# Kernel tuning notes

Measured on AMD Instinct MI355X. Metric: run time of the kernel, lower is better.

## Reference

```python
import jax, jax.numpy as jnp
import numpy as np

K = 1024      # num_embeddings
D = 256       # embedding_dim
BETA = 0.25
DECAY = 0.99
EPS = 1e-05


def setup_inputs() -> dict:
    key = jax.random.key(0)
    k1, k2 = jax.random.split(key)
    z_e = jax.random.normal(k1, (32, D, 32, 32), dtype=jnp.float32)
    embedding = jax.random.normal(k2, (K, D), dtype=jnp.float32)
    ema_cluster_size = jnp.zeros((K,), dtype=jnp.float32)
    ema_w = embedding  # buffer initialized as a clone of the codebook
    return {"z_e": z_e, "embedding": embedding,
            "ema_cluster_size": ema_cluster_size, "ema_w": ema_w}


def reference(z_e, embedding, ema_cluster_size, ema_w):
    B, Dd, H, W = z_e.shape
    # (B, D, H, W) -> (N, D)
    flat_z = jnp.transpose(z_e, (0, 2, 3, 1)).reshape(-1, Dd)

    # L2 distance argmin (||z||^2 + ||e||^2 - 2 z.e)
    dist = (jnp.sum(flat_z * flat_z, axis=1, keepdims=True)
            + jnp.sum(embedding * embedding, axis=1)
            - 2.0 * flat_z @ embedding.T)
    indices = jnp.argmin(dist, axis=1)  # (N,)

    # EMA update (operates on detached values; buffers updated in-place in torch)
    flat_z_sg = jax.lax.stop_gradient(flat_z)
    cluster_size = jax.ops.segment_sum(
        jnp.ones_like(indices, dtype=z_e.dtype), indices, num_segments=K)
    new_ema_cluster_size = DECAY * ema_cluster_size + (1.0 - DECAY) * cluster_size
    dw = jax.ops.segment_sum(flat_z_sg, indices, num_segments=K)  # one_hot.T @ flat_z
    new_ema_w = DECAY * ema_w + (1.0 - DECAY) * dw
    new_embedding = new_ema_w / (new_ema_cluster_size + EPS)[:, None]

    # Gather uses the *updated* codebook (torch copies into the buffer first)
    z_q_flat = new_embedding[indices]                      # (N, D)
    z_q = jnp.transpose(z_q_flat.reshape(B, H, W, Dd), (0, 3, 1, 2))

    # Straight-through estimator + commitment loss
    z_q_st = z_e + jax.lax.stop_gradient(z_q - z_e)
    vq_loss = BETA * jnp.mean((z_e - jax.lax.stop_gradient(z_q)) ** 2)

    return (z_q_st, vq_loss, indices.reshape(B, H, W),
            new_embedding, new_ema_cluster_size, new_ema_w)
```

## Files before the change

### kernel.cpp

```cpp
#include <hip/hip_runtime.h>
#include <stdint.h>

#define N_ROWS 32768
#define K_CODES 1024
#define D_DIM 256
#define NELEM 8388608

#define WS_COUNTS 0
#define WS_ENORM 263168
#define WS_ROWBEST_BYTES 1056768
#define WS_IDX_BYTES 1318912

#define O_ZQ 0
#define O_LOSS 8388608
#define O_IDX 8388609
#define O_EMB 8421377
#define O_CS 8683521
#define O_EMAW 8684545

#define EP_BYTE_OFF 33685520

typedef _Float16 half8 __attribute__((ext_vector_type(8)));
typedef float f32x16 __attribute__((ext_vector_type(16)));

__device__ __forceinline__ unsigned int fenc(float f) {
    unsigned int u = __float_as_uint(f);
    return (u & 0x80000000u) ? ~u : (u | 0x80000000u);
}
__device__ __forceinline__ unsigned long long umin64(unsigned long long a, unsigned long long b) {
    return a < b ? a : b;
}
__device__ __forceinline__ void gll16(const void* g, void* l) {
    __builtin_amdgcn_global_load_lds((const __attribute__((address_space(1))) void*)g,
                                     (__attribute__((address_space(3))) void*)l, 16, 0, 0);
}

__global__ __launch_bounds__(256) void k_init(float* ws) {
    int i = blockIdx.x * 256 + threadIdx.x;
    if (i < 1024) ws[i] = 0.0f;
    unsigned long long* rb = (unsigned long long*)((char*)ws + WS_ROWBEST_BYTES);
    if (i < N_ROWS) rb[i] = 0xFFFFFFFFFFFFFFFFull;
}

__global__ __launch_bounds__(256) void k_conv_e(const float* __restrict__ emb,
                                                _Float16* __restrict__ Ep,
                                                float* __restrict__ enorm) {
    int k = blockIdx.x, d = threadIdx.x;
    float v = emb[k * 256 + d];
    _Float16 h = (_Float16)v;
    _Float16 l = (_Float16)(v - (float)h);
    int s = d >> 3, sub = d & 7;
    Ep[((size_t)s * 1024 + k) * 8 + sub] = h;
    Ep[((size_t)(32 + s) * 1024 + k) * 8 + sub] = l;
    float sq = v * v;
    #pragma unroll
    for (int off = 32; off >= 1; off >>= 1) sq += __shfl_down(sq, off, 64);
    __shared__ float red[4];
    if ((d & 63) == 0) red[d >> 6] = sq;
    __syncthreads();
    if (d == 0) enorm[k] = (red[0] + red[1]) + (red[2] + red[3]);
}

__global__ __launch_bounds__(256) void k_conv_z(const float* __restrict__ z_e,
                                                _Float16* __restrict__ Zp) {
    __shared__ float lt[64 * 68];
    int t = threadIdx.x;
    int hw0 = blockIdx.x * 64, d0 = blockIdx.y * 64, b = blockIdx.z;
    const float* src = z_e + (size_t)b * 262144 + (size_t)d0 * 1024 + hw0;
    int dl = t >> 4, hl = (t & 15) * 4;
    #pragma unroll
    for (int i = 0; i < 4; i++) {
        int d = dl + i * 16;
        float4 v = *(const float4*)(src + (size_t)d * 1024 + hl);
        lt[(hl + 0) * 68 + d] = v.x;
        lt[(hl + 1) * 68 + d] = v.y;
        lt[(hl + 2) * 68 + d] = v.z;
        lt[(hl + 3) * 68 + d] = v.w;
    }
    __syncthreads();
    int hr = t >> 2, seg = t & 3;
    int n = b * 1024 + hw0 + hr;
    int sg0 = (d0 >> 3) + seg * 2;
    half8 hi[2], lo[2];
    #pragma unroll
    for (int p = 0; p < 2; p++) {
        #pragma unroll
        for (int j = 0; j < 8; j++) {
            float v = lt[hr * 68 + seg * 16 + p * 8 + j];
            _Float16 h = (_Float16)v;
            hi[p][j] = h;
            lo[p][j] = (_Float16)(v - (float)h);
        }
    }
    *(half8*)(Zp + ((size_t)(sg0 + 0) * 32768 + n) * 8) = hi[0];
    *(half8*)(Zp + ((size_t)(sg0 + 1) * 32768 + n) * 8) = hi[1];
    *(half8*)(Zp + ((size_t)(32 + sg0) * 32768 + n) * 8) = lo[0];
    *(half8*)(Zp + ((size_t)(33 + sg0) * 32768 + n) * 8) = lo[1];
}

__global__ __launch_bounds__(256) void k_mm(const _Float16* __restrict__ Zp,
                                            const _Float16* __restrict__ Ep,
                                            const float* __restrict__ enorm,
                                            unsigned long long* __restrict__ row_best) {
    __shared__ __align__(16) char smem[32768];
    _Float16* Za = (_Float16*)smem;
    _Float16* Ea = (_Float16*)(smem + 16384);
    unsigned long long* slot = (unsigned long long*)smem;

    int t = threadIdx.x;
    int lane = t & 63, wv = t >> 6;
    int b = blockIdx.x;
    int rt = (b & 7) + ((b >> 6) << 3);
    int ct = (b >> 3) & 7;
    int row0 = rt * 128, code0 = ct * 128;

    int wr = wv >> 1, wc = wv & 1;
    int m31 = lane & 31, ko = lane >> 5;

    f32x16 acc[2][2];
    #pragma unroll
    for (int i = 0; i < 2; i++)
        #pragma unroll
        for (int j = 0; j < 2; j++)
            #pragma unroll
            for (int r = 0; r < 16; r++) acc[i][j][r] = 0.0f;

    const char* zgl = (const char*)Zp + ((size_t)(2 * wv) * 32768 + row0 + lane) * 16;
    const char* egl = (const char*)Ep + ((size_t)(2 * wv) * 1024 + code0 + lane) * 16;
    _Float16* zld = Za + (2 * wv) * 1024;
    _Float16* eld = Ea + (2 * wv) * 1024;

    for (int c = 0; c < 12; c++) {
        int kz = (c < 8) ? c : (c - 8);
        int ge = (c < 4) ? c * 8 : (c < 8) ? (c - 4) * 8 : 32 + (c - 8) * 8;
        const char* zg = zgl + (size_t)kz * 8 * 32768 * 16;
        const char* eg = egl + (size_t)ge * 1024 * 16;
        gll16(zg, zld);
        gll16(zg + 64 * 16, zld + 512);
        gll16(zg + 32768 * 16, zld + 1024);
        gll16(zg + 32768 * 16 + 64 * 16, zld + 1536);
        gll16(eg, eld);
        gll16(eg + 64 * 16, eld + 512);
        gll16(eg + 1024 * 16, eld + 1024);
        gll16(eg + 1024 * 16 + 64 * 16, eld + 1536);
        __syncthreads();
        #pragma unroll
        for (int ks = 0; ks < 4; ks++) {
            int sseg = 2 * ks + ko;
            half8 a0 = *(const half8*)(Za + sseg * 1024 + (wr * 64 + m31) * 8);
            half8 a1 = *(const half8*)(Za + sseg * 1024 + (wr * 64 + 32 + m31) * 8);
            half8 b0 = *(const half8*)(Ea + sseg * 1024 + (wc * 64 + m31) * 8);
            half8 b1 = *(const half8*)(Ea + sseg * 1024 + (wc * 64 + 32 + m31) * 8);
            acc[0][0] = __builtin_amdgcn_mfma_f32_32x32x16_f16(a0, b0, acc[0][0], 0, 0, 0);
            acc[0][1] = __builtin_amdgcn_mfma_f32_32x32x16_f16(a0, b1, acc[0][1], 0, 0, 0);
            acc[1][0] = __builtin_amdgcn_mfma_f32_32x32x16_f16(a1, b0, acc[1][0], 0, 0, 0);
            acc[1][1] = __builtin_amdgcn_mfma_f32_32x32x16_f16(a1, b1, acc[1][1], 0, 0, 0);
        }
        __syncthreads();
    }

    float en0 = enorm[code0 + wc * 64 + m31];
    float en1 = enorm[code0 + wc * 64 + 32 + m31];
    unsigned int col0 = code0 + wc * 64 + m31;
    unsigned int col1 = col0 + 32;

    if (wc == 0) {
        #pragma unroll
        for (int mt = 0; mt < 2; mt++)
            #pragma unroll
            for (int j = 0; j < 16; j++) {
                int row = wr * 64 + mt * 32 + 4 * ko + (j & 3) + 8 * (j >> 2);
                unsigned long long p0 = ((unsigned long long)fenc(en0 - 2.0f * acc[mt][0][j]) << 32) | col0;
                unsigned long long p1 = ((unsigned long long)fenc(en1 - 2.0f * acc[mt][1][j]) << 32) | col1;
                slot[row * 32 + ((m31 + row) & 31)] = umin64(p0, p1);
            }
    }
    __syncthreads();
    if (wc == 1) {
        #pragma unroll
        for (int mt = 0; mt < 2; mt++)
            #pragma unroll
            for (int j = 0; j < 16; j++) {
                int row = wr * 64 + mt * 32 + 4 * ko + (j & 3) + 8 * (j >> 2);
                unsigned long long p0 = ((unsigned long long)fenc(en0 - 2.0f * acc[mt][0][j]) << 32) | col0;
                unsigned long long p1 = ((unsigned long long)fenc(en1 - 2.0f * acc[mt][1][j]) << 32) | col1;
                atomicMin(&slot[row * 32 + ((m31 + row) & 31)], umin64(p0, p1));
            }
    }
    __syncthreads();
    if (t < 128) {
        unsigned long long m = slot[t * 32 + (t & 31)];
        #pragma unroll
        for (int i = 1; i < 32; i++) m = umin64(m, slot[t * 32 + ((i + t) & 31)]);
        atomicMin(&row_best[row0 + t], m);
    }
}

__global__ __launch_bounds__(256) void k_fin_idx(const unsigned long long* __restrict__ rb,
                                                 int* __restrict__ idxs, float* __restrict__ out) {
    int i = blockIdx.x * 256 + threadIdx.x;
    if (i < N_ROWS) {
        int id = (int)(rb[i] & 0xFFFFFFFFull);
        idxs[i] = id;
        out[O_IDX + i] = (float)id;
    }
}

__global__ __launch_bounds__(256) void k_counts(const int* __restrict__ idxs,
                                                float* __restrict__ counts) {
    __shared__ float hist[K_CODES];
    int t = threadIdx.x;
    #pragma unroll
    for (int j = 0; j < 4; j++) hist[j * 256 + t] = 0.0f;
    __syncthreads();
    int n0 = blockIdx.x * 1024;
    #pragma unroll
    for (int i = 0; i < 4; i++) {
        int id = idxs[n0 + i * 256 + t];
        atomicAdd(&hist[id], 1.0f);
    }
    __syncthreads();
    #pragma unroll
    for (int j = 0; j < 4; j++) {
        float h = hist[j * 256 + t];
        if (h != 0.0f) atomicAdd(&counts[j * 256 + t], h);
    }
}

__global__ __launch_bounds__(256) void k_dw(const float* __restrict__ z_e,
                                            const int* __restrict__ idxs,
                                            float* __restrict__ part) {
    __shared__ float acc[K_CODES];
    int t = threadIdx.x;
    int s = blockIdx.x;
    int d = blockIdx.y;
    #pragma unroll
    for (int j = 0; j < 4; j++) acc[j * 256 + t] = 0.0f;
    __syncthreads();
    #pragma unroll
    for (int i = 0; i < 4; i++) {
        int b = s * 4 + i;
        int4 id4 = *(const int4*)(idxs + b * 1024 + t * 4);
        float4 v = *(const float4*)(z_e + (size_t)b * 262144 + (size_t)d * 1024 + t * 4);
        atomicAdd(&acc[id4.x], v.x);
        atomicAdd(&acc[id4.y], v.y);
        atomicAdd(&acc[id4.z], v.z);
        atomicAdd(&acc[id4.w], v.w);
    }
    __syncthreads();
    float* pr = part + ((size_t)s * 256 + d) * 1024;
    #pragma unroll
    for (int j = 0; j < 4; j++) pr[j * 256 + t] = acc[j * 256 + t];
}

__global__ __launch_bounds__(256) void k_red(const float* __restrict__ part,
                                             const float* __restrict__ ema_cs,
                                             const float* __restrict__ ema_w,
                                             const float* __restrict__ counts,
                                             float* __restrict__ out) {
    __shared__ float tile[64 * 69];
    __shared__ float csl[64];
    int t = threadIdx.x;
    int k0 = blockIdx.x * 64, d0 = blockIdx.y * 64;
    int dr = t >> 4, kc = t & 15;
    float4 sum[4] = {};
    for (int s = 0; s < 8; s++) {
        const float* pb = part + ((size_t)s * 256 + d0) * 1024 + k0 + kc * 4;
        #pragma unroll
        for (int q = 0; q < 4; q++) {
            float4 v = *(const float4*)(pb + (size_t)(dr + 16 * q) * 1024);
            sum[q].x += v.x; sum[q].y += v.y; sum[q].z += v.z; sum[q].w += v.w;
        }
    }
    if (t < 64) csl[t] = 0.99f * ema_cs[k0 + t] + 0.01f * counts[k0 + t];
    #pragma unroll
    for (int q = 0; q < 4; q++) {
        float* p = tile + (dr + 16 * q) * 69 + kc * 4;
        p[0] = sum[q].x; p[1] = sum[q].y; p[2] = sum[q].z; p[3] = sum[q].w;
    }
    __syncthreads();
    int kk = t >> 2, dq = t & 3;
    int k = k0 + kk;
    float inv = 1.0f / (csl[kk] + 1e-5f);
    #pragma unroll
    for (int j4 = 0; j4 < 4; j4++) {
        int dd = dq * 16 + j4 * 4;
        size_t kd = (size_t)k * 256 + d0 + dd;
        float4 w = *(const float4*)(ema_w + kd);
        float4 nw;
        nw.x = 0.99f * w.x + 0.01f * tile[(dd + 0) * 69 + kk];
        nw.y = 0.99f * w.y + 0.01f * tile[(dd + 1) * 69 + kk];
        nw.z = 0.99f * w.z + 0.01f * tile[(dd + 2) * 69 + kk];
        nw.w = 0.99f * w.w + 0.01f * tile[(dd + 3) * 69 + kk];
        *(float4*)(out + O_EMAW + kd) = nw;
        float4 ne = {nw.x * inv, nw.y * inv, nw.z * inv, nw.w * inv};
        *(float4*)(out + O_EMB + kd) = ne;
    }
    if (blockIdx.y == 0 && t < 64) out[O_CS + k0 + t] = csl[t];
    if (blockIdx.x == 0 && blockIdx.y == 0 && t == 0) out[O_LOSS] = 0.0f;
}

__global__ __launch_bounds__(256) void k_gather(const float* __restrict__ z_e,
                                                const int* __restrict__ idxs,
                                                float* __restrict__ out) {
    __shared__ float lt[64 * 68];
    __shared__ int sid[64];
    __shared__ float red[4];
    int t = threadIdx.x;
    int hw0 = blockIdx.x * 64, d0 = blockIdx.y * 64, b = blockIdx.z;
    if (t < 64) sid[t] = idxs[b * 1024 + hw0 + t];
    const float* src = z_e + (size_t)b * 262144 + (size_t)d0 * 1024 + hw0;
    int dl = t >> 4, hl = (t & 15) * 4;
    #pragma unroll
    for (int i = 0; i < 4; i++) {
        int d = dl + i * 16;
        float4 v = *(const float4*)(src + (size_t)d * 1024 + hl);
        lt[(hl + 0) * 68 + d] = v.x;
        lt[(hl + 1) * 68 + d] = v.y;
        lt[(hl + 2) * 68 + d] = v.z;
        lt[(hl + 3) * 68 + d] = v.w;
    }
    __syncthreads();
    int r = t >> 2, c = t & 3;
    const float* nrow = out + O_EMB + (size_t)sid[r] * 256 + d0;
    float lacc = 0.0f;
    #pragma unroll
    for (int it = 0; it < 4; it++) {
        int dd = it * 16 + c * 4;
        float4 q = *(const float4*)(nrow + dd);
        float* p = lt + r * 68 + dd;
        float z0 = p[0], z1 = p[1], z2 = p[2], z3 = p[3];
        p[0] = z0 + (q.x - z0);
        p[1] = z1 + (q.y - z1);
        p[2] = z2 + (q.z - z2);
        p[3] = z3 + (q.w - z3);
        float dx = z0 - q.x, dy = z1 - q.y, dz = z2 - q.z, dw4 = z3 - q.w;
        lacc += dx * dx + dy * dy + dz * dz + dw4 * dw4;
    }
    __syncthreads();
    float* dst = out + O_ZQ + (size_t)b * 262144 + (size_t)d0 * 1024 + hw0;
    #pragma unroll
    for (int i = 0; i < 4; i++) {
        int d = dl + i * 16;
        float4 w;
        w.x = lt[(hl + 0) * 68 + d];
        w.y = lt[(hl + 1) * 68 + d];
        w.z = lt[(hl + 2) * 68 + d];
        w.w = lt[(hl + 3) * 68 + d];
        *(float4*)(dst + (size_t)d * 1024 + hl) = w;
    }
    #pragma unroll
    for (int off = 32; off >= 1; off >>= 1) lacc += __shfl_down(lacc, off, 64);
    int lane = t & 63, wv = t >> 6;
    if (lane == 0) red[wv] = lacc;
    __syncthreads();
    if (t == 0) {
        float s = (red[0] + red[1]) + (red[2] + red[3]);
        atomicAdd(out + O_LOSS, s * 2.9802322387695312e-08f);
    }
}

extern "C" void kernel_launch(void* const* d_in, const int* in_sizes, int n_in,
                              void* d_out, int out_size, void* d_ws, size_t ws_size,
                              hipStream_t stream) {
    const float* z_e = (const float*)d_in[0];
    const float* emb = (const float*)d_in[1];
    const float* ema_cs = (const float*)d_in[2];
    const float* ema_w = (const float*)d_in[3];
    float* out = (float*)d_out;
    float* ws = (float*)d_ws;

    float* counts = ws + WS_COUNTS;
    float* enorm = ws + WS_ENORM;
    unsigned long long* row_best = (unsigned long long*)((char*)d_ws + WS_ROWBEST_BYTES);
    int* idxs = (int*)((char*)d_ws + WS_IDX_BYTES);

    _Float16* Zp = (_Float16*)d_out;
    _Float16* Ep = (_Float16*)((char*)d_out + EP_BYTE_OFF);
    float* part = (float*)d_out;

    k_init<<<128, 256, 0, stream>>>(ws);
    k_conv_e<<<1024, 256, 0, stream>>>(emb, Ep, enorm);
    k_conv_z<<<dim3(16, 4, 32), 256, 0, stream>>>(z_e, Zp);
    k_mm<<<2048, 256, 0, stream>>>(Zp, Ep, enorm, row_best);
    k_fin_idx<<<128, 256, 0, stream>>>(row_best, idxs, out);
    k_counts<<<32, 256, 0, stream>>>(idxs, counts);
    k_dw<<<dim3(8, 256), 256, 0, stream>>>(z_e, idxs, part);
    k_red<<<dim3(16, 4), 256, 0, stream>>>(part, ema_cs, ema_w, counts, out);
    k_gather<<<dim3(16, 4, 32), 256, 0, stream>>>(z_e, idxs, out);
}
```

Before: 255.0 us.

## Drop LDS staging in distance GEMM; load fragments directly with register prefetch

```diff
diff --git a/kernel.cpp b/kernel.cpp
--- a/kernel.cpp
+++ b/kernel.cpp
@@ -29,10 +29,6 @@
 }
 __device__ __forceinline__ unsigned long long umin64(unsigned long long a, unsigned long long b) {
     return a < b ? a : b;
-}
-__device__ __forceinline__ void gll16(const void* g, void* l) {
-    __builtin_amdgcn_global_load_lds((const __attribute__((address_space(1))) void*)g,
-                                     (__attribute__((address_space(3))) void*)l, 16, 0, 0);
 }
 
 __global__ __launch_bounds__(256) void k_init(float* ws) {
@@ -102,20 +98,20 @@
                                             const _Float16* __restrict__ Ep,
                                             const float* __restrict__ enorm,
                                             unsigned long long* __restrict__ row_best) {
-    __shared__ __align__(16) char smem[32768];
-    _Float16* Za = (_Float16*)smem;
-    _Float16* Ea = (_Float16*)(smem + 16384);
-    unsigned long long* slot = (unsigned long long*)smem;
-
     int t = threadIdx.x;
     int lane = t & 63, wv = t >> 6;
     int b = blockIdx.x;
-    int rt = (b & 7) + ((b >> 6) << 3);
-    int ct = (b >> 3) & 7;
-    int row0 = rt * 128, code0 = ct * 128;
-
-    int wr = wv >> 1, wc = wv & 1;
+    int rt = (b & 7) + ((b >> 7) << 3);
+    int ct = (b >> 3) & 15;
+    int row0 = rt * 256 + wv * 64;
+    int code0 = ct * 64;
     int m31 = lane & 31, ko = lane >> 5;
+
+    const char* ebase = (const char*)Ep + ((size_t)ko * 1024 + code0 + m31) * 16;
+    const char* zbase = (const char*)Zp + ((size_t)ko * 32768 + row0 + m31) * 16;
+
+    constexpr int ZB[12] = {0, 8, 16, 24, 32, 40, 48, 56, 0, 8, 16, 24};
+    constexpr int EB[12] = {0, 8, 16, 24, 0, 8, 16, 24, 32, 40, 48, 56};
 
     f32x16 acc[2][2];
     #pragma unroll
@@ -125,74 +121,49 @@
             #pragma unroll
             for (int r = 0; r < 16; r++) acc[i][j][r] = 0.0f;
 
-    const char* zgl = (const char*)Zp + ((size_t)(2 * wv) * 32768 + row0 + lane) * 16;
-    const char* egl = (const char*)Ep + ((size_t)(2 * wv) * 1024 + code0 + lane) * 16;
-    _Float16* zld = Za + (2 * wv) * 1024;
-    _Float16* eld = Ea + (2 * wv) * 1024;
-
-    for (int c = 0; c < 12; c++) {
-        int kz = (c < 8) ? c : (c - 8);
-        int ge = (c < 4) ? c * 8 : (c < 8) ? (c - 4) * 8 : 32 + (c - 8) * 8;
-        const char* zg = zgl + (size_t)kz * 8 * 32768 * 16;
-        const char* eg = egl + (size_t)ge * 1024 * 16;
-        gll16(zg, zld);
-        gll16(zg + 64 * 16, zld + 512);
-        gll16(zg + 32768 * 16, zld + 1024);
-        gll16(zg + 32768 * 16 + 64 * 16, zld + 1536);
-        gll16(eg, eld);
-        gll16(eg + 64 * 16, eld + 512);
-        gll16(eg + 1024 * 16, eld + 1024);
-        gll16(eg + 1024 * 16 + 64 * 16, eld + 1536);
-        __syncthreads();
-        #pragma unroll
-        for (int ks = 0; ks < 4; ks++) {
-            int sseg = 2 * ks + ko;
-            half8 a0 = *(const half8*)(Za + sseg * 1024 + (wr * 64 + m31) * 8);
-            half8 a1 = *(const half8*)(Za + sseg * 1024 + (wr * 64 + 32 + m31) * 8);
-            half8 b0 = *(const half8*)(Ea + sseg * 1024 + (wc * 64 + m31) * 8);
-            half8 b1 = *(const half8*)(Ea + sseg * 1024 + (wc * 64 + 32 + m31) * 8);
-            acc[0][0] = __builtin_amdgcn_mfma_f32_32x32x16_f16(a0, b0, acc[0][0], 0, 0, 0);
-            acc[0][1] = __builtin_amdgcn_mfma_f32_32x32x16_f16(a0, b1, acc[0][1], 0, 0, 0);
-            acc[1][0] = __builtin_amdgcn_mfma_f32_32x32x16_f16(a1, b0, acc[1][0], 0, 0, 0);
-            acc[1][1] = __builtin_amdgcn_mfma_f32_32x32x16_f16(a1, b1, acc[1][1], 0, 0, 0);
+#define LDA(c, s, mt) (*(const half8*)(ebase + (((size_t)(EB[c] + 2 * (s))) * 1024 + (mt) * 32) * 16))
+#define LDB(c, s, nt) (*(const half8*)(zbase + (((size_t)(ZB[c] + 2 * (s))) * 32768 + (nt) * 32) * 16))
+
+    half8 a0 = LDA(0, 0, 0), a1 = LDA(0, 0, 1);
+    half8 b0 = LDB(0, 0, 0), b1 = LDB(0, 0, 1);
+    #pragma unroll
+    for (int i = 0; i < 48; i++) {
+        half8 na0, na1, nb0, nb1;
+        if (i < 47) {
+            int c2 = (i + 1) >> 2, s2 = (i + 1) & 3;
+            na0 = LDA(c2, s2, 0); na1 = LDA(c2, s2, 1);
+            nb0 = LDB(c2, s2, 0); nb1 = LDB(c2, s2, 1);
         }
-        __syncthreads();
-    }
-
-    float en0 = enorm[code0 + wc * 64 + m31];
-    float en1 = enorm[code0 + wc * 64 + 32 + m31];
-    unsigned int col0 = code0 + wc * 64 + m31;
-    unsigned int col1 = col0 + 32;
-
-    if (wc == 0) {
+        acc[0][0] = __builtin_amdgcn_mfma_f32_32x32x16_f16(a0, b0, acc[0][0], 0, 0, 0);
+        acc[0][1] = __builtin_amdgcn_mfma_f32_32x32x16_f16(a0, b1, acc[0][1], 0, 0, 0);
+        acc[1][0] = __builtin_amdgcn_mfma_f32_32x32x16_f16(a1, b0, acc[1][0], 0, 0, 0);
+        acc[1][1] = __builtin_amdgcn_mfma_f32_32x32x16_f16(a1, b1, acc[1][1], 0, 0, 0);
+        a0 = na0; a1 = na1; b0 = nb0; b1 = nb1;
+    }
+#undef LDA
+#undef LDB
+
+    float en_a[32];
+    #pragma unroll
+    for (int mt = 0; mt < 2; mt++)
+        #pragma unroll
+        for (int r = 0; r < 16; r++)
+            en_a[mt * 16 + r] = enorm[code0 + mt * 32 + 4 * ko + (r & 3) + 8 * (r >> 2)];
+
+    #pragma unroll
+    for (int nt = 0; nt < 2; nt++) {
+        unsigned long long best = 0xFFFFFFFFFFFFFFFFull;
         #pragma unroll
         for (int mt = 0; mt < 2; mt++)
             #pragma unroll
-            for (int j = 0; j < 16; j++) {
-                int row = wr * 64 + mt * 32 + 4 * ko + (j & 3) + 8 * (j >> 2);
-                unsigned long long p0 = ((unsigned long long)fenc(en0 - 2.0f * acc[mt][0][j]) << 32) | col0;
-                unsigned long long p1 = ((unsigned long long)fenc(en1 - 2.0f * acc[mt][1][j]) << 32) | col1;
-                slot[row * 32 + ((m31 + row) & 31)] = umin64(p0, p1);
+            for (int r = 0; r < 16; r++) {
+                unsigned int code = code0 + mt * 32 + 4 * ko + (r & 3) + 8 * (r >> 2);
+                float dist = en_a[mt * 16 + r] - 2.0f * acc[mt][nt][r];
+                unsigned long long pk = ((unsigned long long)fenc(dist) << 32) | code;
+                best = umin64(best, pk);
             }
-    }
-    __syncthreads();
-    if (wc == 1) {
-        #pragma unroll
-        for (int mt = 0; mt < 2; mt++)
-            #pragma unroll
-            for (int j = 0; j < 16; j++) {
-                int row = wr * 64 + mt * 32 + 4 * ko + (j & 3) + 8 * (j >> 2);
-                unsigned long long p0 = ((unsigned long long)fenc(en0 - 2.0f * acc[mt][0][j]) << 32) | col0;
-                unsigned long long p1 = ((unsigned long long)fenc(en1 - 2.0f * acc[mt][1][j]) << 32) | col1;
-                atomicMin(&slot[row * 32 + ((m31 + row) & 31)], umin64(p0, p1));
-            }
-    }
-    __syncthreads();
-    if (t < 128) {
-        unsigned long long m = slot[t * 32 + (t & 31)];
-        #pragma unroll
-        for (int i = 1; i < 32; i++) m = umin64(m, slot[t * 32 + ((i + t) & 31)]);
-        atomicMin(&row_best[row0 + t], m);
+        best = umin64(best, __shfl_xor(best, 32, 64));
+        if (ko == 0) atomicMin(&row_best[row0 + nt * 32 + m31], best);
     }
 }
 
```

New measurement: 277.4 us. 1.09x slower.

## Compute commitment loss algebraically and drop z_e reread in gather

Applied to the files above, without the earlier changes.

```diff
diff --git a/kernel.cpp b/kernel.cpp
--- a/kernel.cpp
+++ b/kernel.cpp
@@ -7,6 +7,7 @@
 #define NELEM 8388608
 
 #define WS_COUNTS 0
+#define WS_LOSS 1030
 #define WS_ENORM 263168
 #define WS_ROWBEST_BYTES 1056768
 #define WS_IDX_BYTES 1318912
@@ -37,7 +38,7 @@
 
 __global__ __launch_bounds__(256) void k_init(float* ws) {
     int i = blockIdx.x * 256 + threadIdx.x;
-    if (i < 1024) ws[i] = 0.0f;
+    if (i < 2048) ws[i] = 0.0f;
     unsigned long long* rb = (unsigned long long*)((char*)ws + WS_ROWBEST_BYTES);
     if (i < N_ROWS) rb[i] = 0xFFFFFFFFFFFFFFFFull;
 }
@@ -62,16 +63,20 @@
 }
 
 __global__ __launch_bounds__(256) void k_conv_z(const float* __restrict__ z_e,
-                                                _Float16* __restrict__ Zp) {
+                                                _Float16* __restrict__ Zp,
+                                                float* __restrict__ lossacc) {
     __shared__ float lt[64 * 68];
+    __shared__ float red[4];
     int t = threadIdx.x;
     int hw0 = blockIdx.x * 64, d0 = blockIdx.y * 64, b = blockIdx.z;
     const float* src = z_e + (size_t)b * 262144 + (size_t)d0 * 1024 + hw0;
     int dl = t >> 4, hl = (t & 15) * 4;
+    float sq = 0.0f;
     #pragma unroll
     for (int i = 0; i < 4; i++) {
         int d = dl + i * 16;
         float4 v = *(const float4*)(src + (size_t)d * 1024 + hl);
+        sq += v.x * v.x + v.y * v.y + v.z * v.z + v.w * v.w;
         lt[(hl + 0) * 68 + d] = v.x;
         lt[(hl + 1) * 68 + d] = v.y;
         lt[(hl + 2) * 68 + d] = v.z;
@@ -96,6 +101,11 @@
     *(half8*)(Zp + ((size_t)(sg0 + 1) * 32768 + n) * 8) = hi[1];
     *(half8*)(Zp + ((size_t)(32 + sg0) * 32768 + n) * 8) = lo[0];
     *(half8*)(Zp + ((size_t)(33 + sg0) * 32768 + n) * 8) = lo[1];
+    #pragma unroll
+    for (int off = 32; off >= 1; off >>= 1) sq += __shfl_down(sq, off, 64);
+    if ((t & 63) == 0) red[t >> 6] = sq;
+    __syncthreads();
+    if (t == 0) atomicAdd(lossacc, (red[0] + red[1]) + (red[2] + red[3]));
 }
 
 __global__ __launch_bounds__(256) void k_mm(const _Float16* __restrict__ Zp,
@@ -127,8 +137,8 @@
 
     const char* zgl = (const char*)Zp + ((size_t)(2 * wv) * 32768 + row0 + lane) * 16;
     const char* egl = (const char*)Ep + ((size_t)(2 * wv) * 1024 + code0 + lane) * 16;
-    _Float16* zld = Za + (2 * wv) * 1024;
-    _Float16* eld = Ea + (2 * wv) * 1024;
+    _Float16* zld = Za + 2 * wv * 1024;
+    _Float16* eld = Ea + 2 * wv * 1024;
 
     for (int c = 0; c < 12; c++) {
         int kz = (c < 8) ? c : (c - 8);
@@ -197,28 +207,19 @@
 }
 
 __global__ __launch_bounds__(256) void k_fin_idx(const unsigned long long* __restrict__ rb,
-                                                 int* __restrict__ idxs, float* __restrict__ out) {
-    int i = blockIdx.x * 256 + threadIdx.x;
-    if (i < N_ROWS) {
-        int id = (int)(rb[i] & 0xFFFFFFFFull);
-        idxs[i] = id;
-        out[O_IDX + i] = (float)id;
-    }
-}
-
-__global__ __launch_bounds__(256) void k_counts(const int* __restrict__ idxs,
-                                                float* __restrict__ counts) {
+                                                 int* __restrict__ idxs,
+                                                 float* __restrict__ counts,
+                                                 float* __restrict__ out) {
     __shared__ float hist[K_CODES];
     int t = threadIdx.x;
     #pragma unroll
     for (int j = 0; j < 4; j++) hist[j * 256 + t] = 0.0f;
     __syncthreads();
-    int n0 = blockIdx.x * 1024;
-    #pragma unroll
-    for (int i = 0; i < 4; i++) {
-        int id = idxs[n0 + i * 256 + t];
-        atomicAdd(&hist[id], 1.0f);
-    }
+    int i = blockIdx.x * 256 + t;
+    int id = (int)(rb[i] & 0xFFFFFFFFull);
+    idxs[i] = id;
+    out[O_IDX + i] = (float)id;
+    atomicAdd(&hist[id], 1.0f);
     __syncthreads();
     #pragma unroll
     for (int j = 0; j < 4; j++) {
@@ -257,9 +258,12 @@
                                              const float* __restrict__ ema_cs,
                                              const float* __restrict__ ema_w,
                                              const float* __restrict__ counts,
+                                             float* __restrict__ lossacc,
                                              float* __restrict__ out) {
     __shared__ float tile[64 * 69];
     __shared__ float csl[64];
+    __shared__ float craw[64];
+    __shared__ float red[4];
     int t = threadIdx.x;
     int k0 = blockIdx.x * 64, d0 = blockIdx.y * 64;
     int dr = t >> 4, kc = t & 15;
@@ -272,7 +276,11 @@
             sum[q].x += v.x; sum[q].y += v.y; sum[q].z += v.z; sum[q].w += v.w;
         }
     }
-    if (t < 64) csl[t] = 0.99f * ema_cs[k0 + t] + 0.01f * counts[k0 + t];
+    if (t < 64) {
+        float c = counts[k0 + t];
+        craw[t] = c;
+        csl[t] = 0.99f * ema_cs[k0 + t] + 0.01f * c;
+    }
     #pragma unroll
     for (int q = 0; q < 4; q++) {
         float* p = tile + (dr + 16 * q) * 69 + kc * 4;
@@ -282,62 +290,58 @@
     int kk = t >> 2, dq = t & 3;
     int k = k0 + kk;
     float inv = 1.0f / (csl[kk] + 1e-5f);
+    float cr = craw[kk];
+    float lterm = 0.0f;
     #pragma unroll
     for (int j4 = 0; j4 < 4; j4++) {
         int dd = dq * 16 + j4 * 4;
         size_t kd = (size_t)k * 256 + d0 + dd;
         float4 w = *(const float4*)(ema_w + kd);
+        float s0 = tile[(dd + 0) * 69 + kk];
+        float s1 = tile[(dd + 1) * 69 + kk];
+        float s2 = tile[(dd + 2) * 69 + kk];
+        float s3 = tile[(dd + 3) * 69 + kk];
         float4 nw;
-        nw.x = 0.99f * w.x + 0.01f * tile[(dd + 0) * 69 + kk];
-        nw.y = 0.99f * w.y + 0.01f * tile[(dd + 1) * 69 + kk];
-        nw.z = 0.99f * w.z + 0.01f * tile[(dd + 2) * 69 + kk];
-        nw.w = 0.99f * w.w + 0.01f * tile[(dd + 3) * 69 + kk];
+        nw.x = 0.99f * w.x + 0.01f * s0;
+        nw.y = 0.99f * w.y + 0.01f * s1;
+        nw.z = 0.99f * w.z + 0.01f * s2;
+        nw.w = 0.99f * w.w + 0.01f * s3;
         *(float4*)(out + O_EMAW + kd) = nw;
         float4 ne = {nw.x * inv, nw.y * inv, nw.z * inv, nw.w * inv};
         *(float4*)(out + O_EMB + kd) = ne;
+        lterm += ne.x * (cr * ne.x - 2.0f * s0);
+        lterm += ne.y * (cr * ne.y - 2.0f * s1);
+        lterm += ne.z * (cr * ne.z - 2.0f * s2);
+        lterm += ne.w * (cr * ne.w - 2.0f * s3);
     }
     if (blockIdx.y == 0 && t < 64) out[O_CS + k0 + t] = csl[t];
-    if (blockIdx.x == 0 && blockIdx.y == 0 && t == 0) out[O_LOSS] = 0.0f;
-}
-
-__global__ __launch_bounds__(256) void k_gather(const float* __restrict__ z_e,
-                                                const int* __restrict__ idxs,
-                                                float* __restrict__ out) {
+    #pragma unroll
+    for (int off = 32; off >= 1; off >>= 1) lterm += __shfl_down(lterm, off, 64);
+    if ((t & 63) == 0) red[t >> 6] = lterm;
+    __syncthreads();
+    if (t == 0) atomicAdd(lossacc, (red[0] + red[1]) + (red[2] + red[3]));
+}
+
+__global__ __launch_bounds__(256) void k_bcast(const int* __restrict__ idxs,
+                                               const float* __restrict__ lossacc,
+                                               float* __restrict__ out) {
     __shared__ float lt[64 * 68];
     __shared__ int sid[64];
-    __shared__ float red[4];
     int t = threadIdx.x;
     int hw0 = blockIdx.x * 64, d0 = blockIdx.y * 64, b = blockIdx.z;
     if (t < 64) sid[t] = idxs[b * 1024 + hw0 + t];
-    const float* src = z_e + (size_t)b * 262144 + (size_t)d0 * 1024 + hw0;
-    int dl = t >> 4, hl = (t & 15) * 4;
-    #pragma unroll
-    for (int i = 0; i < 4; i++) {
-        int d = dl + i * 16;
-        float4 v = *(const float4*)(src + (size_t)d * 1024 + hl);
-        lt[(hl + 0) * 68 + d] = v.x;
-        lt[(hl + 1) * 68 + d] = v.y;
-        lt[(hl + 2) * 68 + d] = v.z;
-        lt[(hl + 3) * 68 + d] = v.w;
-    }
     __syncthreads();
     int r = t >> 2, c = t & 3;
     const float* nrow = out + O_EMB + (size_t)sid[r] * 256 + d0;
-    float lacc = 0.0f;
     #pragma unroll
     for (int it = 0; it < 4; it++) {
         int dd = it * 16 + c * 4;
         float4 q = *(const float4*)(nrow + dd);
         float* p = lt + r * 68 + dd;
-        float z0 = p[0], z1 = p[1], z2 = p[2], z3 = p[3];
-        p[0] = z0 + (q.x - z0);
-        p[1] = z1 + (q.y - z1);
-        p[2] = z2 + (q.z - z2);
-        p[3] = z3 + (q.w - z3);
-        float dx = z0 - q.x, dy = z1 - q.y, dz = z2 - q.z, dw4 = z3 - q.w;
-        lacc += dx * dx + dy * dy + dz * dz + dw4 * dw4;
-    }
-    __syncthreads();
+        p[0] = q.x; p[1] = q.y; p[2] = q.z; p[3] = q.w;
+    }
+    __syncthreads();
+    int dl = t >> 4, hl = (t & 15) * 4;
     float* dst = out + O_ZQ + (size_t)b * 262144 + (size_t)d0 * 1024 + hw0;
     #pragma unroll
     for (int i = 0; i < 4; i++) {
@@ -349,15 +353,8 @@
         w.w = lt[(hl + 3) * 68 + d];
         *(float4*)(dst + (size_t)d * 1024 + hl) = w;
     }
-    #pragma unroll
-    for (int off = 32; off >= 1; off >>= 1) lacc += __shfl_down(lacc, off, 64);
-    int lane = t & 63, wv = t >> 6;
-    if (lane == 0) red[wv] = lacc;
-    __syncthreads();
-    if (t == 0) {
-        float s = (red[0] + red[1]) + (red[2] + red[3]);
-        atomicAdd(out + O_LOSS, s * 2.9802322387695312e-08f);
-    }
+    if (blockIdx.x == 0 && blockIdx.y == 0 && blockIdx.z == 0 && t == 0)
+        out[O_LOSS] = lossacc[0] * 2.9802322387695312e-08f;
 }
 
 extern "C" void kernel_launch(void* const* d_in, const int* in_sizes, int n_in,
@@ -371,6 +368,7 @@
     float* ws = (float*)d_ws;
 
     float* counts = ws + WS_COUNTS;
+    float* lossacc = ws + WS_LOSS;
     float* enorm = ws + WS_ENORM;
     unsigned long long* row_best = (unsigned long long*)((char*)d_ws + WS_ROWBEST_BYTES);
     int* idxs = (int*)((char*)d_ws + WS_IDX_BYTES);
@@ -381,11 +379,10 @@
 
     k_init<<<128, 256, 0, stream>>>(ws);
     k_conv_e<<<1024, 256, 0, stream>>>(emb, Ep, enorm);
-    k_conv_z<<<dim3(16, 4, 32), 256, 0, stream>>>(z_e, Zp);
+    k_conv_z<<<dim3(16, 4, 32), 256, 0, stream>>>(z_e, Zp, lossacc);
     k_mm<<<2048, 256, 0, stream>>>(Zp, Ep, enorm, row_best);
-    k_fin_idx<<<128, 256, 0, stream>>>(row_best, idxs, out);
-    k_counts<<<32, 256, 0, stream>>>(idxs, counts);
+    k_fin_idx<<<128, 256, 0, stream>>>(row_best, idxs, counts, out);
     k_dw<<<dim3(8, 256), 256, 0, stream>>>(z_e, idxs, part);
-    k_red<<<dim3(16, 4), 256, 0, stream>>>(part, ema_cs, ema_w, counts, out);
-    k_gather<<<dim3(16, 4, 32), 256, 0, stream>>>(z_e, idxs, out);
-}
+    k_red<<<dim3(16, 4), 256, 0, stream>>>(part, ema_cs, ema_w, counts, lossacc, out);
+    k_bcast<<<dim3(16, 4, 32), 256, 0, stream>>>(idxs, lossacc, out);
+}
```

Result: faster. 240.5 us (-5.7%).
